# Optimization experiments

Hardware: AMD Instinct MI355X
Metric: run time of the kernel (lower is better)

Reference implementation:

```python
import jax, jax.numpy as jnp
import numpy as np

N, D, C = 131072, 256, 1000
EPS = 1e-6


def setup_inputs() -> dict:
    key = jax.random.key(0)
    k1, k2, k3, k4 = jax.random.split(key, 4)
    feats = jax.random.normal(k1, (N, D), dtype=jnp.float32)
    pseudo_lbls = jax.random.randint(k2, (N,), 0, C)
    src_proto = jax.random.normal(k3, (C, D), dtype=jnp.float32)
    # uniform in [0.5, 1.5) to keep the Mahalanobis denominator well-conditioned
    src_proto_cov = jax.random.uniform(k4, (C, D), dtype=jnp.float32) + 0.5
    return {"feats": feats, "pseudo_lbls": pseudo_lbls,
            "src_proto": src_proto, "src_proto_cov": src_proto_cov}


def reference(feats, pseudo_lbls, src_proto, src_proto_cov):
    # Fused scatter-mean over classes (replaces the python loop over unique labels).
    num_classes, feat_dim = src_proto.shape
    counts = jax.ops.segment_sum(jnp.ones((feats.shape[0],), feats.dtype),
                                 pseudo_lbls, num_segments=num_classes)  # [C]
    sums = jax.ops.segment_sum(feats, pseudo_lbls, num_segments=num_classes)  # [C, D]
    means = sums / jnp.maximum(counts, 1.0)[:, None]                      # [C, D]
    present = counts > 0                                                  # [C]
    # GSSLoss: mean over the [n_uniq, D] elements of (mean - proto)^2 / (cov + eps)
    per_elem = (means - src_proto) ** 2 / (src_proto_cov + EPS)           # [C, D]
    per_elem = jnp.where(present[:, None], per_elem, 0.0)
    n_present = jnp.sum(present.astype(feats.dtype))
    loss = jnp.sum(per_elem) / (n_present * feat_dim)
    return loss
```

## Files before the change

### kernel.cpp

```cpp
#include <hip/hip_runtime.h>

#define EPS 1e-6f
#define CAP 512


__global__ void bucket_kernel(const int* __restrict__ lbls,
                              int* __restrict__ counts,
                              int* __restrict__ rowidx, int n) {
    int i = blockIdx.x * blockDim.x + threadIdx.x;
    if (i < n) {
        int l = lbls[i];
        int pos = atomicAdd(&counts[l], 1);
        if (pos < CAP) rowidx[(size_t)l * CAP + pos] = i;
    }
}

__global__ __launch_bounds__(256)
void partial_kernel(const float* __restrict__ feats,
                    const int* __restrict__ rowidx,
                    const int* __restrict__ counts,
                    float* __restrict__ partials, int d) {
    int blk  = blockIdx.x;
    int c    = blk >> 1;
    int j    = blk & 1;
    int t    = threadIdx.x;
    int wave = t >> 6;
    int col4 = t & 63;
    int stride4 = d >> 2;

    int cnt = counts[c];
    if (cnt > CAP) cnt = CAP;
    int half = (cnt + 1) >> 1;
    int lo = j ? half : 0;
    int hi = j ? cnt : half;
    int m  = hi - lo;

    __shared__ int sidx[(CAP + 1) / 2 + 1];
    for (int i = t; i < m; i += 256)
        sidx[i] = rowidx[(size_t)c * CAP + lo + i];
    __syncthreads();

    const float4* f4 = (const float4*)feats;
    float4 acc = make_float4(0.f, 0.f, 0.f, 0.f);

    int i = wave;
    for (; i + 28 < m; i += 32) {
        int r0 = sidx[i];
        int r1 = sidx[i + 4];
        int r2 = sidx[i + 8];
        int r3 = sidx[i + 12];
        int r4 = sidx[i + 16];
        int r5 = sidx[i + 20];
        int r6 = sidx[i + 24];
        int r7 = sidx[i + 28];
        float4 v0 = f4[(size_t)r0 * stride4 + col4];
        float4 v1 = f4[(size_t)r1 * stride4 + col4];
        float4 v2 = f4[(size_t)r2 * stride4 + col4];
        float4 v3 = f4[(size_t)r3 * stride4 + col4];
        float4 v4 = f4[(size_t)r4 * stride4 + col4];
        float4 v5 = f4[(size_t)r5 * stride4 + col4];
        float4 v6 = f4[(size_t)r6 * stride4 + col4];
        float4 v7 = f4[(size_t)r7 * stride4 + col4];
        acc.x += ((v0.x + v1.x) + (v2.x + v3.x)) + ((v4.x + v5.x) + (v6.x + v7.x));
        acc.y += ((v0.y + v1.y) + (v2.y + v3.y)) + ((v4.y + v5.y) + (v6.y + v7.y));
        acc.z += ((v0.z + v1.z) + (v2.z + v3.z)) + ((v4.z + v5.z) + (v6.z + v7.z));
        acc.w += ((v0.w + v1.w) + (v2.w + v3.w)) + ((v4.w + v5.w) + (v6.w + v7.w));
    }
    for (; i < m; i += 4) {
        int r0 = sidx[i];
        float4 v0 = f4[(size_t)r0 * stride4 + col4];
        acc.x += v0.x; acc.y += v0.y; acc.z += v0.z; acc.w += v0.w;
    }

    __shared__ float4 sacc[256];
    sacc[t] = acc;
    __syncthreads();

    if (t < 64) {
        float4 a0 = sacc[t], a1 = sacc[t + 64], a2 = sacc[t + 128], a3 = sacc[t + 192];
        float4 r;
        r.x = (a0.x + a1.x) + (a2.x + a3.x);
        r.y = (a0.y + a1.y) + (a2.y + a3.y);
        r.z = (a0.z + a1.z) + (a2.z + a3.z);
        r.w = (a0.w + a1.w) + (a2.w + a3.w);
        ((float4*)partials)[(size_t)blk * stride4 + t] = r;
    }
}

__global__ __launch_bounds__(256)
void finalize_kernel(const float* __restrict__ partials,
                     const int* __restrict__ counts,
                     const float* __restrict__ proto,
                     const float* __restrict__ cov,
                     float* __restrict__ loss_acc,
                     float* __restrict__ npres_acc,
                     int* __restrict__ done,
                     float* __restrict__ out, int c_total, int d) {
    int c = blockIdx.x;
    int t = threadIdx.x;
    size_t idx = (size_t)c * d + t;
    float a = partials[(size_t)(2 * c) * d + t] + partials[(size_t)(2 * c + 1) * d + t];
    int cnt = counts[c];
    float present = (cnt > 0) ? 1.0f : 0.0f;
    float mean = a / fmaxf((float)cnt, 1.0f);
    float diff = mean - proto[idx];
    float pe = present * diff * diff / (cov[idx] + EPS);

    for (int off = 32; off > 0; off >>= 1)
        pe += __shfl_down(pe, off, 64);
    __shared__ float s[4];
    if ((t & 63) == 0) s[t >> 6] = pe;
    __syncthreads();
    if (t == 0) {
        atomicAdd(loss_acc, (s[0] + s[1]) + (s[2] + s[3]));
        atomicAdd(npres_acc, present);
        __threadfence();
        int prev = atomicAdd(done, 1);
        if (prev == c_total - 1) {
            float L = atomicAdd(loss_acc, 0.0f);
            float P = atomicAdd(npres_acc, 0.0f);
            out[0] = L / (P * (float)d);
        }
    }
}

extern "C" void kernel_launch(void* const* d_in, const int* in_sizes, int n_in,
                              void* d_out, int out_size, void* d_ws, size_t ws_size,
                              hipStream_t stream) {
    const float* feats = (const float*)d_in[0];
    const int*   lbls  = (const int*)d_in[1];
    const float* proto = (const float*)d_in[2];
    const float* cov   = (const float*)d_in[3];

    int n_rows = in_sizes[1];
    int d      = in_sizes[0] / n_rows;
    int c      = in_sizes[2] / d;

    int*   counts    = (int*)d_ws;
    float* loss_acc  = (float*)d_ws + c;
    float* npres_acc = loss_acc + 1;
    int*   done      = (int*)d_ws + c + 2;
    int*   rowidx    = (int*)d_ws + c + 3;
    float* partials  = (float*)d_ws + c + 3 + (size_t)c * CAP;

    hipMemsetAsync(d_ws, 0, ((size_t)c + 3) * sizeof(int), stream);

    int nb = (n_rows + 255) / 256;
    bucket_kernel<<<nb, 256, 0, stream>>>(lbls, counts, rowidx, n_rows);
    partial_kernel<<<2 * c, 256, 0, stream>>>(feats, rowidx, counts, partials, d);
    finalize_kernel<<<c, 256, 0, stream>>>(partials, counts, proto, cov,
                                           loss_acc, npres_acc, done,
                                           (float*)d_out, c, d);
}
```

Baseline: 273.5 us.

## Fuse partial gather-sum and finalize into one per-class kernel

The separate partial-sum and finalize kernels are merged into one kernel with one block per class. Each block gathers all of its rows, reduces them, then computes the Mahalanobis term and does the atomic loss accumulation directly. This removes a kernel launch and the partials round trip through global memory. In exchange the grid is halved, from 2000 blocks to 1000 blocks, which lowers parallelism for the memory-bound gather on a GPU with many CUs.

```diff
diff --git a/kernel.cpp b/kernel.cpp
--- a/kernel.cpp
+++ b/kernel.cpp
@@ -16,28 +16,27 @@
 }
 
 __global__ __launch_bounds__(256)
-void partial_kernel(const float* __restrict__ feats,
-                    const int* __restrict__ rowidx,
-                    const int* __restrict__ counts,
-                    float* __restrict__ partials, int d) {
-    int blk  = blockIdx.x;
-    int c    = blk >> 1;
-    int j    = blk & 1;
+void fused_kernel(const float* __restrict__ feats,
+                  const int* __restrict__ rowidx,
+                  const int* __restrict__ counts,
+                  const float* __restrict__ proto,
+                  const float* __restrict__ cov,
+                  float* __restrict__ loss_acc,
+                  float* __restrict__ npres_acc,
+                  int* __restrict__ done,
+                  float* __restrict__ out, int c_total, int d) {
+    int c    = blockIdx.x;
     int t    = threadIdx.x;
     int wave = t >> 6;
     int col4 = t & 63;
     int stride4 = d >> 2;
 
     int cnt = counts[c];
-    if (cnt > CAP) cnt = CAP;
-    int half = (cnt + 1) >> 1;
-    int lo = j ? half : 0;
-    int hi = j ? cnt : half;
-    int m  = hi - lo;
+    int m   = cnt > CAP ? CAP : cnt;
 
-    __shared__ int sidx[(CAP + 1) / 2 + 1];
+    __shared__ int sidx[CAP];
     for (int i = t; i < m; i += 256)
-        sidx[i] = rowidx[(size_t)c * CAP + lo + i];
+        sidx[i] = rowidx[(size_t)c * CAP + i];
     __syncthreads();
 
     const float4* f4 = (const float4*)feats;
@@ -83,43 +82,31 @@
         r.y = (a0.y + a1.y) + (a2.y + a3.y);
         r.z = (a0.z + a1.z) + (a2.z + a3.z);
         r.w = (a0.w + a1.w) + (a2.w + a3.w);
-        ((float4*)partials)[(size_t)blk * stride4 + t] = r;
-    }
-}
 
-__global__ __launch_bounds__(256)
-void finalize_kernel(const float* __restrict__ partials,
-                     const int* __restrict__ counts,
-                     const float* __restrict__ proto,
-                     const float* __restrict__ cov,
-                     float* __restrict__ loss_acc,
-                     float* __restrict__ npres_acc,
-                     int* __restrict__ done,
-                     float* __restrict__ out, int c_total, int d) {
-    int c = blockIdx.x;
-    int t = threadIdx.x;
-    size_t idx = (size_t)c * d + t;
-    float a = partials[(size_t)(2 * c) * d + t] + partials[(size_t)(2 * c + 1) * d + t];
-    int cnt = counts[c];
-    float present = (cnt > 0) ? 1.0f : 0.0f;
-    float mean = a / fmaxf((float)cnt, 1.0f);
-    float diff = mean - proto[idx];
-    float pe = present * diff * diff / (cov[idx] + EPS);
+        float present = (cnt > 0) ? 1.0f : 0.0f;
+        float inv = 1.0f / fmaxf((float)cnt, 1.0f);
+        float4 p4 = ((const float4*)proto)[(size_t)c * stride4 + t];
+        float4 c4 = ((const float4*)cov)[(size_t)c * stride4 + t];
+        float dx = r.x * inv - p4.x;
+        float dy = r.y * inv - p4.y;
+        float dz = r.z * inv - p4.z;
+        float dw = r.w * inv - p4.w;
+        float pe = present * ((dx * dx / (c4.x + EPS) + dy * dy / (c4.y + EPS)) +
+                              (dz * dz / (c4.z + EPS) + dw * dw / (c4.w + EPS)));
 
-    for (int off = 32; off > 0; off >>= 1)
-        pe += __shfl_down(pe, off, 64);
-    __shared__ float s[4];
-    if ((t & 63) == 0) s[t >> 6] = pe;
-    __syncthreads();
-    if (t == 0) {
-        atomicAdd(loss_acc, (s[0] + s[1]) + (s[2] + s[3]));
-        atomicAdd(npres_acc, present);
-        __threadfence();
-        int prev = atomicAdd(done, 1);
-        if (prev == c_total - 1) {
-            float L = atomicAdd(loss_acc, 0.0f);
-            float P = atomicAdd(npres_acc, 0.0f);
-            out[0] = L / (P * (float)d);
+        for (int off = 32; off > 0; off >>= 1)
+            pe += __shfl_down(pe, off, 64);
+
+        if (t == 0) {
+            atomicAdd(loss_acc, pe);
+            atomicAdd(npres_acc, present);
+            __threadfence();
+            int prev = atomicAdd(done, 1);
+            if (prev == c_total - 1) {
+                float L = atomicAdd(loss_acc, 0.0f);
+                float P = atomicAdd(npres_acc, 0.0f);
+                out[0] = L / (P * (float)d);
+            }
         }
     }
 }
@@ -141,14 +128,12 @@
     float* npres_acc = loss_acc + 1;
     int*   done      = (int*)d_ws + c + 2;
     int*   rowidx    = (int*)d_ws + c + 3;
-    float* partials  = (float*)d_ws + c + 3 + (size_t)c * CAP;
 
     hipMemsetAsync(d_ws, 0, ((size_t)c + 3) * sizeof(int), stream);
 
     int nb = (n_rows + 255) / 256;
     bucket_kernel<<<nb, 256, 0, stream>>>(lbls, counts, rowidx, n_rows);
-    partial_kernel<<<2 * c, 256, 0, stream>>>(feats, rowidx, counts, partials, d);
-    finalize_kernel<<<c, 256, 0, stream>>>(partials, counts, proto, cov,
-                                           loss_acc, npres_acc, done,
-                                           (float*)d_out, c, d);
+    fused_kernel<<<c, 256, 0, stream>>>(feats, rowidx, counts, proto, cov,
+                                        loss_acc, npres_acc, done,
+                                        (float*)d_out, c, d);
 }
```

New measurement: 274.1 us. No clear change (+0.2%).

## Replace bucket-gather with streaming LDS-atomic segmented sum over column slices

Applied to the files above, without the earlier changes.

Drops the label bucketing pass and the indexed gather. A single streaming kernel now reads feats contiguously, split into 32-column slices and row chunks. Each block accumulates per-class sums with shared-memory float atomics, using a class-dependent rotation to spread bank conflicts, and writes per-chunk partials that finalize reduces over 32 chunks. This also removes the CAP truncation. In exchange it adds heavy LDS atomic contention, 128KB of shared memory per block (one block per CU), and a larger partials buffer of about 32 MB to write and re-read.

```diff
diff --git a/kernel.cpp b/kernel.cpp
--- a/kernel.cpp
+++ b/kernel.cpp
@@ -1,89 +1,78 @@
 #include <hip/hip_runtime.h>
 
 #define EPS 1e-6f
-#define CAP 512
+#define MAX_C 1000
+#define W 32
+#define NCHUNKS 32
+#define SBLK 1024
 
 
-__global__ void bucket_kernel(const int* __restrict__ lbls,
-                              int* __restrict__ counts,
-                              int* __restrict__ rowidx, int n) {
-    int i = blockIdx.x * blockDim.x + threadIdx.x;
-    if (i < n) {
-        int l = lbls[i];
-        int pos = atomicAdd(&counts[l], 1);
-        if (pos < CAP) rowidx[(size_t)l * CAP + pos] = i;
-    }
-}
-
-__global__ __launch_bounds__(256)
-void partial_kernel(const float* __restrict__ feats,
-                    const int* __restrict__ rowidx,
-                    const int* __restrict__ counts,
-                    float* __restrict__ partials, int d) {
-    int blk  = blockIdx.x;
-    int c    = blk >> 1;
-    int j    = blk & 1;
+__global__ __launch_bounds__(SBLK)
+void stream_kernel(const float* __restrict__ feats,
+                   const int* __restrict__ lbls,
+                   float* __restrict__ partials,
+                   int* __restrict__ counts,
+                   int n, int d, int nslices, int rpc, int c_total) {
+    int slice = blockIdx.x % nslices;
+    int chunk = blockIdx.x / nslices;
     int t    = threadIdx.x;
     int wave = t >> 6;
-    int col4 = t & 63;
-    int stride4 = d >> 2;
+    int lane = t & 63;
+    int rg   = lane >> 3;
+    int cg   = lane & 7;
 
-    int cnt = counts[c];
-    if (cnt > CAP) cnt = CAP;
-    int half = (cnt + 1) >> 1;
-    int lo = j ? half : 0;
-    int hi = j ? cnt : half;
-    int m  = hi - lo;
-
-    __shared__ int sidx[(CAP + 1) / 2 + 1];
-    for (int i = t; i < m; i += 256)
-        sidx[i] = rowidx[(size_t)c * CAP + lo + i];
+    __shared__ float smem[MAX_C * W];
+    int cW = c_total * W;
+    for (int i = t; i < cW; i += SBLK) smem[i] = 0.0f;
     __syncthreads();
 
+    int base = chunk * rpc;
+    int rend = base + rpc;
+    if (rend > n) rend = n;
+
     const float4* f4 = (const float4*)feats;
-    float4 acc = make_float4(0.f, 0.f, 0.f, 0.f);
+    int stride4 = d >> 2;
+    int colbase4 = slice * (W >> 2);
+    int colbase  = slice * W;
 
-    int i = wave;
-    for (; i + 28 < m; i += 32) {
-        int r0 = sidx[i];
-        int r1 = sidx[i + 4];
-        int r2 = sidx[i + 8];
-        int r3 = sidx[i + 12];
-        int r4 = sidx[i + 16];
-        int r5 = sidx[i + 20];
-        int r6 = sidx[i + 24];
-        int r7 = sidx[i + 28];
-        float4 v0 = f4[(size_t)r0 * stride4 + col4];
-        float4 v1 = f4[(size_t)r1 * stride4 + col4];
-        float4 v2 = f4[(size_t)r2 * stride4 + col4];
-        float4 v3 = f4[(size_t)r3 * stride4 + col4];
-        float4 v4 = f4[(size_t)r4 * stride4 + col4];
-        float4 v5 = f4[(size_t)r5 * stride4 + col4];
-        float4 v6 = f4[(size_t)r6 * stride4 + col4];
-        float4 v7 = f4[(size_t)r7 * stride4 + col4];
-        acc.x += ((v0.x + v1.x) + (v2.x + v3.x)) + ((v4.x + v5.x) + (v6.x + v7.x));
-        acc.y += ((v0.y + v1.y) + (v2.y + v3.y)) + ((v4.y + v5.y) + (v6.y + v7.y));
-        acc.z += ((v0.z + v1.z) + (v2.z + v3.z)) + ((v4.z + v5.z) + (v6.z + v7.z));
-        acc.w += ((v0.w + v1.w) + (v2.w + v3.w)) + ((v4.w + v5.w) + (v6.w + v7.w));
+    for (int r0 = base + wave * 16; r0 < rend; r0 += 16 * (SBLK / 64)) {
+        int rA = r0 + rg;
+        int rB = rA + 8;
+        bool okA = rA < rend, okB = rB < rend;
+        int lA = 0, lB = 0;
+        float4 vA = make_float4(0.f, 0.f, 0.f, 0.f);
+        float4 vB = vA;
+        if (okA) { lA = lbls[rA]; vA = f4[(size_t)rA * stride4 + colbase4 + cg]; }
+        if (okB) { lB = lbls[rB]; vB = f4[(size_t)rB * stride4 + colbase4 + cg]; }
+
+        if (slice == 0 && cg == 0) {
+            if (okA) atomicAdd(&counts[lA], 1);
+            if (okB) atomicAdd(&counts[lB], 1);
+        }
+
+        if (okA) {
+            int lc = cg << 2, b = lA * W;
+            atomicAdd(&smem[b + ((lc + 0 + lA) & (W - 1))], vA.x);
+            atomicAdd(&smem[b + ((lc + 1 + lA) & (W - 1))], vA.y);
+            atomicAdd(&smem[b + ((lc + 2 + lA) & (W - 1))], vA.z);
+            atomicAdd(&smem[b + ((lc + 3 + lA) & (W - 1))], vA.w);
+        }
+        if (okB) {
+            int lc = cg << 2, b = lB * W;
+            atomicAdd(&smem[b + ((lc + 0 + lB) & (W - 1))], vB.x);
+            atomicAdd(&smem[b + ((lc + 1 + lB) & (W - 1))], vB.y);
+            atomicAdd(&smem[b + ((lc + 2 + lB) & (W - 1))], vB.z);
+            atomicAdd(&smem[b + ((lc + 3 + lB) & (W - 1))], vB.w);
+        }
     }
-    for (; i < m; i += 4) {
-        int r0 = sidx[i];
-        float4 v0 = f4[(size_t)r0 * stride4 + col4];
-        acc.x += v0.x; acc.y += v0.y; acc.z += v0.z; acc.w += v0.w;
-    }
-
-    __shared__ float4 sacc[256];
-    sacc[t] = acc;
     __syncthreads();
 
-    if (t < 64) {
-        float4 a0 = sacc[t], a1 = sacc[t + 64], a2 = sacc[t + 128], a3 = sacc[t + 192];
-        float4 r;
-        r.x = (a0.x + a1.x) + (a2.x + a3.x);
-        r.y = (a0.y + a1.y) + (a2.y + a3.y);
-        r.z = (a0.z + a1.z) + (a2.z + a3.z);
-        r.w = (a0.w + a1.w) + (a2.w + a3.w);
-        ((float4*)partials)[(size_t)blk * stride4 + t] = r;
+    float* pbase = partials + (size_t)chunk * c_total * d;
+    for (int i = t; i < cW; i += SBLK) {
+        int cls  = i >> 5;
+        int phys = i & (W - 1);
+        int lc   = (phys - cls) & (W - 1);
+        pbase[(size_t)cls * d + colbase + lc] = smem[i];
     }
 }
 
@@ -95,11 +84,16 @@
                      float* __restrict__ loss_acc,
                      float* __restrict__ npres_acc,
                      int* __restrict__ done,
-                     float* __restrict__ out, int c_total, int d) {
+                     float* __restrict__ out, int c_total, int d, int nchunks) {
     int c = blockIdx.x;
     int t = threadIdx.x;
     size_t idx = (size_t)c * d + t;
-    float a = partials[(size_t)(2 * c) * d + t] + partials[(size_t)(2 * c + 1) * d + t];
+    size_t cstride = (size_t)c_total * d;
+
+    float a = 0.0f;
+    for (int k = 0; k < nchunks; ++k)
+        a += partials[(size_t)k * cstride + idx];
+
     int cnt = counts[c];
     float present = (cnt > 0) ? 1.0f : 0.0f;
     float mean = a / fmaxf((float)cnt, 1.0f);
@@ -140,15 +134,15 @@
     float* loss_acc  = (float*)d_ws + c;
     float* npres_acc = loss_acc + 1;
     int*   done      = (int*)d_ws + c + 2;
-    int*   rowidx    = (int*)d_ws + c + 3;
-    float* partials  = (float*)d_ws + c + 3 + (size_t)c * CAP;
+    float* partials  = (float*)d_ws + c + 3;
 
     hipMemsetAsync(d_ws, 0, ((size_t)c + 3) * sizeof(int), stream);
 
-    int nb = (n_rows + 255) / 256;
-    bucket_kernel<<<nb, 256, 0, stream>>>(lbls, counts, rowidx, n_rows);
-    partial_kernel<<<2 * c, 256, 0, stream>>>(feats, rowidx, counts, partials, d);
+    int nslices = d / W;
+    int rpc = (n_rows + NCHUNKS - 1) / NCHUNKS;
+    stream_kernel<<<nslices * NCHUNKS, SBLK, 0, stream>>>(
+        feats, lbls, partials, counts, n_rows, d, nslices, rpc, c);
     finalize_kernel<<<c, 256, 0, stream>>>(partials, counts, proto, cov,
                                            loss_acc, npres_acc, done,
-                                           (float*)d_out, c, d);
+                                           (float*)d_out, c, d, NCHUNKS);
 }
```

Measured after the change: 381.2 us. +39.4%, slower.
